# Performance work log

Hardware: AMD Instinct MI355X
Metric: run time of the kernel (lower is better)

## Reference

```python
import jax, jax.numpy as jnp
import numpy as np

H = 1024      # hidden_size
NH = 16       # num_heads
HD = 128      # head_dim
ID = NH * HD  # inner_dim = 2048
EPS = 1e-6


def setup_inputs() -> dict:
    key = jax.random.key(0)
    ks = jax.random.split(key, 8)
    n = lambda k, shape, sc=1.0: jax.random.normal(k, shape, dtype=jnp.float32) * sc
    return {
        "x": n(ks[0], (1, H)),
        "rnn_state": n(ks[1], (1, NH, HD, HD)),
        "conv_state": n(ks[2], (1, 3 * ID, 3)),
        # learned parameters (nn.Linear stores W as [out_features, in_features])
        "W_qkv": n(ks[3], (3 * ID, H), 0.02),
        "W_z": n(ks[4], (ID, H), 0.02),
        "W_a": n(ks[5], (NH, H), 0.02),
        "norm_w": jnp.ones((HD,), jnp.float32),
        "W_out": n(ks[6], (H, ID), 0.02),
    }


def reference(x, rnn_state, conv_state, W_qkv, W_z, W_a, norm_w, W_out):
    # QKV projection: [1, 3*ID]
    qkv = x @ W_qkv.T
    q, k, v = jnp.split(qkv, 3, axis=-1)
    q = q.reshape(-1, NH, HD)
    k = k.reshape(-1, NH, HD)
    v = v.reshape(-1, NH, HD)

    # per-head scalar decay in (0,1): [1, NH, 1, 1]
    decay = jax.nn.sigmoid(x @ W_a.T)[:, :, None, None]

    # outer product k \otimes v: [1, NH, HD, HD]
    kv = k[..., :, None] * v[..., None, :]
    new_state = rnn_state * decay + kv

    # query readout: [1, NH, HD]
    y = jnp.einsum('bhd,bhde->bhe', q, new_state)

    # RMSNorm over head_dim
    y = y * jax.lax.rsqrt(jnp.mean(y * y, axis=-1, keepdims=True) + EPS) * norm_w
    y = y.reshape(-1, ID)

    # silu-gated combine and output projection
    z = x @ W_z.T
    y = y * (z * jax.nn.sigmoid(z))
    out = y @ W_out.T
    return (out, new_state, conv_state)
```

## Files before the change

### kernel.cpp

```cpp
#include <hip/hip_runtime.h>
#include <math.h>

#define H    1024
#define NH   16
#define HD   128
#define ID   2048
#define NROWS_A (3*ID + ID + NH)
#define MATVEC_BLOCKS (NROWS_A / 4)
#define CONV_FLOATS (3 * ID * 3)
#define CONV_BLOCKS (CONV_FLOATS / 4 / 256)
#define EPS 1e-6f

__device__ __forceinline__ float waveReduceSum(float v) {
#pragma unroll
    for (int off = 32; off > 0; off >>= 1) v += __shfl_down(v, off, 64);
    return v;
}

__global__ __launch_bounds__(256) void matvec_qkvza(
    const float* __restrict__ x,
    const float* __restrict__ Wqkv,
    const float* __restrict__ Wz,
    const float* __restrict__ Wa,
    const float* __restrict__ conv,
    float* __restrict__ conv_out,
    float* __restrict__ ws_qkv,
    float* __restrict__ ws_zsig,
    float* __restrict__ ws_decay)
{
    if (blockIdx.x >= MATVEC_BLOCKS) {
        const int i = (blockIdx.x - MATVEC_BLOCKS) * 256 + threadIdx.x;
        ((float4*)conv_out)[i] = ((const float4*)conv)[i];
        return;
    }

    const int wave = threadIdx.x >> 6;
    const int lane = threadIdx.x & 63;
    const int r = blockIdx.x * 4 + wave;

    const float* row;
    if (r < 3 * ID)           row = Wqkv + (size_t)r * H;
    else if (r < 3 * ID + ID) row = Wz   + (size_t)(r - 3 * ID) * H;
    else                      row = Wa   + (size_t)(r - 3 * ID - ID) * H;

    const float4* row4 = (const float4*)row;
    const float4* x4   = (const float4*)x;

    float acc = 0.f;
#pragma unroll
    for (int t = 0; t < 4; ++t) {
        float4 w  = row4[lane + 64 * t];
        float4 xv = x4[lane + 64 * t];
        acc += w.x * xv.x + w.y * xv.y + w.z * xv.z + w.w * xv.w;
    }
    acc = waveReduceSum(acc);
    if (lane == 0) {
        if (r < 3 * ID) {
            ws_qkv[r] = acc;
        } else if (r < 3 * ID + ID) {
            const float sig = 1.f / (1.f + expf(-acc));
            ws_zsig[r - 3 * ID] = acc * sig;
        } else {
            ws_decay[r - 3 * ID - ID] = 1.f / (1.f + expf(-acc));
        }
    }
}

__global__ __launch_bounds__(256) void state_update(
    const float* __restrict__ state_in,
    const float* __restrict__ ws_qkv,
    const float* __restrict__ ws_decay,
    float* __restrict__ state_out,
    float* __restrict__ ws_ypart)
{
    const int h  = blockIdx.x >> 4;
    const int s  = blockIdx.x & 15;
    const int dd = threadIdx.x >> 5;
    const int c  = threadIdx.x & 31;
    const int d  = s * 8 + dd;

    const float decay = ws_decay[h];
    const float qd = ws_qkv[h * HD + d];
    const float kd = ws_qkv[ID + h * HD + d];
    const float4 vv = ((const float4*)(ws_qkv + 2 * ID + h * HD))[c];

    const float4* sin4 = (const float4*)(state_in  + (size_t)h * HD * HD);
    float4*       sout = (float4*)(state_out + (size_t)h * HD * HD);

    float4 sv = sin4[d * 32 + c];
    float4 sn;
    sn.x = sv.x * decay + kd * vv.x;
    sn.y = sv.y * decay + kd * vv.y;
    sn.z = sv.z * decay + kd * vv.z;
    sn.w = sv.w * decay + kd * vv.w;
    sout[d * 32 + c] = sn;

    __shared__ float part[8][HD];
    part[dd][4 * c + 0] = qd * sn.x;
    part[dd][4 * c + 1] = qd * sn.y;
    part[dd][4 * c + 2] = qd * sn.z;
    part[dd][4 * c + 3] = qd * sn.w;
    __syncthreads();

    const int t = threadIdx.x;
    if (t < HD) {
        float y = 0.f;
#pragma unroll
        for (int d2 = 0; d2 < 8; ++d2) y += part[d2][t];
        ws_ypart[(h * 16 + s) * HD + t] = y;
    }
}

__global__ __launch_bounds__(256) void gate_out(
    const float* __restrict__ ws_ypart,
    const float* __restrict__ ws_zsig,
    const float* __restrict__ normw,
    const float* __restrict__ Wout,
    float* __restrict__ out)
{
    __shared__ float gated[ID];
    const int t = threadIdx.x;
    {
        const int h  = t >> 4;
        const int eb = (t & 15) * 8;
        float y[8];
#pragma unroll
        for (int j = 0; j < 8; ++j) y[j] = 0.f;
#pragma unroll 4
        for (int s = 0; s < 16; ++s) {
            const float4* yp = (const float4*)(ws_ypart + (h * 16 + s) * HD + eb);
            float4 a0 = yp[0], a1 = yp[1];
            y[0] += a0.x; y[1] += a0.y; y[2] += a0.z; y[3] += a0.w;
            y[4] += a1.x; y[5] += a1.y; y[6] += a1.z; y[7] += a1.w;
        }
        float ss = 0.f;
#pragma unroll
        for (int j = 0; j < 8; ++j) ss += y[j] * y[j];
        ss += __shfl_xor(ss, 1, 16);
        ss += __shfl_xor(ss, 2, 16);
        ss += __shfl_xor(ss, 4, 16);
        ss += __shfl_xor(ss, 8, 16);
        const float scale = rsqrtf(ss * (1.f / HD) + EPS);
#pragma unroll
        for (int j = 0; j < 8; ++j) {
            const int e = eb + j;
            gated[h * HD + e] = y[j] * scale * normw[e] * ws_zsig[h * HD + e];
        }
    }
    __syncthreads();
    {
        const int wave = t >> 6;
        const int lane = t & 63;
        const int r = blockIdx.x * 4 + wave;
        const float4* row4 = (const float4*)(Wout + (size_t)r * ID);
        const float4* g4   = (const float4*)gated;
        float acc = 0.f;
#pragma unroll
        for (int i = 0; i < 8; ++i) {
            float4 wv = row4[lane + 64 * i];
            float4 gv = g4[lane + 64 * i];
            acc += wv.x * gv.x + wv.y * gv.y + wv.z * gv.z + wv.w * gv.w;
        }
        acc = waveReduceSum(acc);
        if (lane == 0) out[r] = acc;
    }
}

extern "C" void kernel_launch(void* const* d_in, const int* in_sizes, int n_in,
                              void* d_out, int out_size, void* d_ws, size_t ws_size,
                              hipStream_t stream) {
    const float* x     = (const float*)d_in[0];
    const float* state = (const float*)d_in[1];
    const float* conv  = (const float*)d_in[2];
    const float* Wqkv  = (const float*)d_in[3];
    const float* Wz    = (const float*)d_in[4];
    const float* Wa    = (const float*)d_in[5];
    const float* normw = (const float*)d_in[6];
    const float* Wout  = (const float*)d_in[7];

    float* out       = (float*)d_out;
    float* new_state = out + H;
    float* conv_out  = new_state + (size_t)NH * HD * HD;

    float* ws       = (float*)d_ws;
    float* ws_qkv   = ws;
    float* ws_zsig  = ws + 6144;
    float* ws_decay = ws + 8192;
    float* ws_ypart = ws + 8208;

    matvec_qkvza<<<MATVEC_BLOCKS + CONV_BLOCKS, 256, 0, stream>>>(
        x, Wqkv, Wz, Wa, conv, conv_out, ws_qkv, ws_zsig, ws_decay);
    state_update<<<NH * 16, 256, 0, stream>>>(
        state, ws_qkv, ws_decay, new_state, ws_ypart);
    gate_out<<<H / 4, 256, 0, stream>>>(
        ws_ypart, ws_zsig, normw, Wout, out);
}
```

Baseline: 18.84 us.

## Fuse state update, norm, gating and output projection into one per-head kernel

Merges the state-update and gate/output-projection kernels into one kernel that uses 64 blocks of 1024 threads, four per head. Each block recomputes its head's full state readout and RMSNorm, writes only its quarter of the new state, and projects its head slice onto 256 output rows, accumulating into out with atomicAdd. Out is zeroed by the first conv-copy block of the first kernel. This removes one launch and the ypart workspace round trip, but each block reads the whole head state (4x redundant reads), there are far fewer blocks, and the atomic accumulation makes the output summation order nondeterministic.

New measurement: 21.47 us. 13.9% more time.

```diff
diff --git a/kernel.cpp b/kernel.cpp
--- a/kernel.cpp
+++ b/kernel.cpp
@@ -10,6 +10,8 @@
 #define CONV_FLOATS (3 * ID * 3)
 #define CONV_BLOCKS (CONV_FLOATS / 4 / 256)
 #define EPS 1e-6f
+#define SPLIT 4
+#define K2_BLOCKS (NH * SPLIT)
 
 __device__ __forceinline__ float waveReduceSum(float v) {
 #pragma unroll
@@ -24,13 +26,19 @@
     const float* __restrict__ Wa,
     const float* __restrict__ conv,
     float* __restrict__ conv_out,
+    float* __restrict__ out,
     float* __restrict__ ws_qkv,
     float* __restrict__ ws_zsig,
     float* __restrict__ ws_decay)
 {
     if (blockIdx.x >= MATVEC_BLOCKS) {
-        const int i = (blockIdx.x - MATVEC_BLOCKS) * 256 + threadIdx.x;
+        const int cb = blockIdx.x - MATVEC_BLOCKS;
+        const int i = cb * 256 + threadIdx.x;
         ((float4*)conv_out)[i] = ((const float4*)conv)[i];
+        if (cb == 0) {
+            float4 z4 = {0.f, 0.f, 0.f, 0.f};
+            ((float4*)out)[threadIdx.x] = z4;
+        }
         return;
     }
 
@@ -66,103 +74,103 @@
     }
 }
 
-__global__ __launch_bounds__(256) void state_update(
+__global__ __launch_bounds__(1024) void head_update_out(
     const float* __restrict__ state_in,
     const float* __restrict__ ws_qkv,
     const float* __restrict__ ws_decay,
+    const float* __restrict__ ws_zsig,
+    const float* __restrict__ normw,
+    const float* __restrict__ Wout,
     float* __restrict__ state_out,
-    float* __restrict__ ws_ypart)
+    float* __restrict__ out)
 {
-    const int h  = blockIdx.x >> 4;
-    const int s  = blockIdx.x & 15;
-    const int dd = threadIdx.x >> 5;
-    const int c  = threadIdx.x & 31;
-    const int d  = s * 8 + dd;
+    const int h  = blockIdx.x >> 2;
+    const int p  = blockIdx.x & 3;
+    const int t  = threadIdx.x;
+    const int wv = t >> 6;
+    const int lane = t & 63;
+    const int d  = t >> 3;
+    const int g  = t & 7;
+
+    __shared__ float part[16][HD];
+    __shared__ float gated[HD];
+    __shared__ float red2[2];
 
     const float decay = ws_decay[h];
     const float qd = ws_qkv[h * HD + d];
     const float kd = ws_qkv[ID + h * HD + d];
-    const float4 vv = ((const float4*)(ws_qkv + 2 * ID + h * HD))[c];
 
     const float4* sin4 = (const float4*)(state_in  + (size_t)h * HD * HD);
     float4*       sout = (float4*)(state_out + (size_t)h * HD * HD);
-
-    float4 sv = sin4[d * 32 + c];
-    float4 sn;
-    sn.x = sv.x * decay + kd * vv.x;
-    sn.y = sv.y * decay + kd * vv.y;
-    sn.z = sv.z * decay + kd * vv.z;
-    sn.w = sv.w * decay + kd * vv.w;
-    sout[d * 32 + c] = sn;
-
-    __shared__ float part[8][HD];
-    part[dd][4 * c + 0] = qd * sn.x;
-    part[dd][4 * c + 1] = qd * sn.y;
-    part[dd][4 * c + 2] = qd * sn.z;
-    part[dd][4 * c + 3] = qd * sn.w;
+    const float4* v4   = (const float4*)(ws_qkv + 2 * ID + h * HD);
+
+    const bool do_write = (wv >> 2) == p;
+
+    float4 acc[4];
+#pragma unroll
+    for (int k = 0; k < 4; ++k) {
+        const int c = g + 8 * k;
+        const float4 vv = v4[c];
+        const float4 sv = sin4[d * 32 + c];
+        float4 sn;
+        sn.x = sv.x * decay + kd * vv.x;
+        sn.y = sv.y * decay + kd * vv.y;
+        sn.z = sv.z * decay + kd * vv.z;
+        sn.w = sv.w * decay + kd * vv.w;
+        if (do_write) sout[d * 32 + c] = sn;
+        acc[k].x = qd * sn.x;
+        acc[k].y = qd * sn.y;
+        acc[k].z = qd * sn.z;
+        acc[k].w = qd * sn.w;
+    }
+#pragma unroll
+    for (int k = 0; k < 4; ++k) {
+#pragma unroll
+        for (int off = 8; off < 64; off <<= 1) {
+            acc[k].x += __shfl_xor(acc[k].x, off, 64);
+            acc[k].y += __shfl_xor(acc[k].y, off, 64);
+            acc[k].z += __shfl_xor(acc[k].z, off, 64);
+            acc[k].w += __shfl_xor(acc[k].w, off, 64);
+        }
+    }
+    if (lane < 8) {
+#pragma unroll
+        for (int k = 0; k < 4; ++k)
+            ((float4*)part[wv])[lane + 8 * k] = acc[k];
+    }
     __syncthreads();
 
-    const int t = threadIdx.x;
+    float y = 0.f;
     if (t < HD) {
-        float y = 0.f;
-#pragma unroll
-        for (int d2 = 0; d2 < 8; ++d2) y += part[d2][t];
-        ws_ypart[(h * 16 + s) * HD + t] = y;
-    }
-}
-
-__global__ __launch_bounds__(256) void gate_out(
-    const float* __restrict__ ws_ypart,
-    const float* __restrict__ ws_zsig,
-    const float* __restrict__ normw,
-    const float* __restrict__ Wout,
-    float* __restrict__ out)
-{
-    __shared__ float gated[ID];
-    const int t = threadIdx.x;
+#pragma unroll
+        for (int w2 = 0; w2 < 16; ++w2) y += part[w2][t];
+        float s2 = y * y;
+#pragma unroll
+        for (int off = 1; off < 64; off <<= 1) s2 += __shfl_xor(s2, off, 64);
+        if (lane == 0) red2[t >> 6] = s2;
+    }
+    __syncthreads();
+    if (t < HD) {
+        const float scale = rsqrtf((red2[0] + red2[1]) * (1.f / HD) + EPS);
+        gated[t] = y * scale * normw[t] * ws_zsig[h * HD + t];
+    }
+    __syncthreads();
+
     {
-        const int h  = t >> 4;
-        const int eb = (t & 15) * 8;
-        float y[8];
-#pragma unroll
-        for (int j = 0; j < 8; ++j) y[j] = 0.f;
-#pragma unroll 4
-        for (int s = 0; s < 16; ++s) {
-            const float4* yp = (const float4*)(ws_ypart + (h * 16 + s) * HD + eb);
-            float4 a0 = yp[0], a1 = yp[1];
-            y[0] += a0.x; y[1] += a0.y; y[2] += a0.z; y[3] += a0.w;
-            y[4] += a1.x; y[5] += a1.y; y[6] += a1.z; y[7] += a1.w;
-        }
-        float ss = 0.f;
-#pragma unroll
-        for (int j = 0; j < 8; ++j) ss += y[j] * y[j];
-        ss += __shfl_xor(ss, 1, 16);
-        ss += __shfl_xor(ss, 2, 16);
-        ss += __shfl_xor(ss, 4, 16);
-        ss += __shfl_xor(ss, 8, 16);
-        const float scale = rsqrtf(ss * (1.f / HD) + EPS);
-#pragma unroll
-        for (int j = 0; j < 8; ++j) {
-            const int e = eb + j;
-            gated[h * HD + e] = y[j] * scale * normw[e] * ws_zsig[h * HD + e];
-        }
-    }
-    __syncthreads();
-    {
-        const int wave = t >> 6;
-        const int lane = t & 63;
-        const int r = blockIdx.x * 4 + wave;
-        const float4* row4 = (const float4*)(Wout + (size_t)r * ID);
+        const int r  = p * 256 + (t >> 2);
+        const int jq = t & 3;
+        const float4* wrow = (const float4*)(Wout + (size_t)r * ID + h * HD);
         const float4* g4   = (const float4*)gated;
-        float acc = 0.f;
+        float a = 0.f;
 #pragma unroll
         for (int i = 0; i < 8; ++i) {
-            float4 wv = row4[lane + 64 * i];
-            float4 gv = g4[lane + 64 * i];
-            acc += wv.x * gv.x + wv.y * gv.y + wv.z * gv.z + wv.w * gv.w;
-        }
-        acc = waveReduceSum(acc);
-        if (lane == 0) out[r] = acc;
+            const float4 w4 = wrow[jq * 8 + i];
+            const float4 gv = g4[jq * 8 + i];
+            a += w4.x * gv.x + w4.y * gv.y + w4.z * gv.z + w4.w * gv.w;
+        }
+        a += __shfl_xor(a, 1, 64);
+        a += __shfl_xor(a, 2, 64);
+        if (jq == 0) atomicAdd(&out[r], a);
     }
 }
 
@@ -186,12 +194,9 @@
     float* ws_qkv   = ws;
     float* ws_zsig  = ws + 6144;
     float* ws_decay = ws + 8192;
-    float* ws_ypart = ws + 8208;
 
     matvec_qkvza<<<MATVEC_BLOCKS + CONV_BLOCKS, 256, 0, stream>>>(
-        x, Wqkv, Wz, Wa, conv, conv_out, ws_qkv, ws_zsig, ws_decay);
-    state_update<<<NH * 16, 256, 0, stream>>>(
-        state, ws_qkv, ws_decay, new_state, ws_ypart);
-    gate_out<<<H / 4, 256, 0, stream>>>(
-        ws_ypart, ws_zsig, normw, Wout, out);
-}
+        x, Wqkv, Wz, Wa, conv, conv_out, out, ws_qkv, ws_zsig, ws_decay);
+    head_update_out<<<K2_BLOCKS, 1024, 0, stream>>>(
+        state, ws_qkv, ws_decay, ws_zsig, normw, Wout, new_state, out);
+}
```
